# Performance work log

Hardware: AMD Instinct MI355X
Metric: run time of the kernel (lower is better)

Reference implementation:

```python
import jax, jax.numpy as jnp
import numpy as np

HEADS = 8
DIM_HEAD = 64


def setup_inputs() -> dict:
    key = jax.random.key(0)
    ks = jax.random.split(key, 5)
    dim = 512
    dim_inner = HEADS * DIM_HEAD
    return {
        "fmap": jax.random.normal(ks[0], (8, dim, 32, 32), dtype=jnp.float32),
        "gamma": jnp.ones((dim,), dtype=jnp.float32),
        "wq": jax.random.normal(ks[1], (dim_inner, dim), dtype=jnp.float32) * 0.05,
        "wv": jax.random.normal(ks[2], (dim_inner, dim), dtype=jnp.float32) * 0.05,
        "null_kv": jax.random.normal(ks[3], (2, HEADS, DIM_HEAD), dtype=jnp.float32),
        "wo": jax.random.normal(ks[4], (dim, dim_inner), dtype=jnp.float32) * 0.05,
    }


def reference(fmap, gamma, wq, wv, null_kv, wo):
    b, c, H, W = fmap.shape
    h, d = HEADS, DIM_HEAD
    n = H * W
    scale = d ** (-0.5)

    # ChannelRMSNorm: F.normalize over channel dim * sqrt(dim) * gamma
    l2 = jnp.sqrt(jnp.sum(fmap * fmap, axis=1, keepdims=True))
    x = fmap / jnp.maximum(l2, 1e-12) * (c ** 0.5) * gamma[None, :, None, None]

    # 1x1 convs as channel matmuls -> [b, h, n, d]
    def proj(w):
        t = jnp.einsum('bcxy,oc->boxy', x, w)          # [b, h*d, H, W]
        return t.reshape(b, h, d, n).transpose(0, 1, 3, 2)  # [b, h, n, d]

    q = proj(wq)
    v = proj(wv)
    k = q  # dot_product=False -> to_k is None, k = q

    # prepend null kv token
    nk = jnp.broadcast_to(null_kv[0][None, :, None, :], (b, h, 1, d))
    nv = jnp.broadcast_to(null_kv[1][None, :, None, :], (b, h, 1, d))
    k = jnp.concatenate([nk, k], axis=2)  # [b, h, n+1, d]
    v = jnp.concatenate([nv, v], axis=2)

    # negative squared L2 distance score: -(|q|^2 + |k|^2 - 2 q.k)
    q_sq = jnp.sum(q * q, axis=-1)  # [b, h, n]
    k_sq = jnp.sum(k * k, axis=-1)  # [b, h, n+1]
    qk = jnp.einsum('bhid,bhjd->bhij', q, k)
    sim = -(q_sq[..., :, None] + k_sq[..., None, :] - 2.0 * qk) * scale

    attn = jax.nn.softmax(sim, axis=-1)
    out = jnp.einsum('bhij,bhjd->bhid', attn, v)  # [b, h, n, d]

    out = out.transpose(0, 1, 3, 2).reshape(b, h * d, H, W)
    return jnp.einsum('boxy,co->bcxy', out, wo)
```

## Files before the change

kernel.cpp:

```cpp
#include <hip/hip_runtime.h>
#include <hip/hip_bf16.h>

#define DEV static __device__ __forceinline__

typedef __bf16 bf16x8 __attribute__((ext_vector_type(8)));
typedef float f32x4 __attribute__((ext_vector_type(4)));
typedef float f32x16 __attribute__((ext_vector_type(16)));
typedef unsigned u32x4 __attribute__((ext_vector_type(4)));
typedef unsigned short u16x8 __attribute__((ext_vector_type(8)));
typedef unsigned short u16x4 __attribute__((ext_vector_type(4)));

DEV unsigned short f2bf(float f) {
  unsigned u = __builtin_bit_cast(unsigned, f);
  u += 0x7fffu + ((u >> 16) & 1u);
  return (unsigned short)(u >> 16);
}
DEV float bf2f(unsigned short s) {
  return __builtin_bit_cast(float, (unsigned)s << 16);
}
DEV f32x4 mfma16(bf16x8 a, bf16x8 b, f32x4 c) {
  return __builtin_amdgcn_mfma_f32_16x16x32_bf16(a, b, c, 0, 0, 0);
}
DEV f32x16 mfma32(bf16x8 a, bf16x8 b, f32x16 c) {
  return __builtin_amdgcn_mfma_f32_32x32x16_bf16(a, b, c, 0, 0, 0);
}
DEV bf16x8 ld8(const unsigned short* p) {
  return __builtin_bit_cast(bf16x8, *(const u16x8*)p);
}
DEV void gload16(const unsigned short* g, unsigned short* l) {
  auto* g1 = reinterpret_cast<const __attribute__((address_space(1))) unsigned int*>(
      reinterpret_cast<uintptr_t>(g));
  auto* l3 = reinterpret_cast<__attribute__((address_space(3))) unsigned int*>(
      reinterpret_cast<uintptr_t>(l));
  __builtin_amdgcn_global_load_lds(g1, l3, 16, 0, 0);
}

__global__ __launch_bounds__(256) void prep_k(const float* __restrict__ fmap,
                                              const float* __restrict__ gamma,
                                              const float* __restrict__ wq,
                                              const float* __restrict__ wv,
                                              const float* __restrict__ wo,
                                              unsigned short* __restrict__ xt,
                                              unsigned short* __restrict__ wqb,
                                              unsigned short* __restrict__ wvb,
                                              unsigned short* __restrict__ wob) {
  int bid = blockIdx.x, tid = threadIdx.x;
  if (bid >= 256) {
    int t4 = bid - 256;
    int g = t4 >> 5;
    const float* src = (g == 0) ? wq : (g == 1) ? wv : wo;
    unsigned short* dst = (g == 0) ? wqb : (g == 1) ? wvb : wob;
    int base = (t4 & 31) * 1024 + tid;
    const float4* s = (const float4*)src;
#pragma unroll
    for (int i = 0; i < 4; ++i) {
      int idx = base + i * 256;
      float4 a = s[idx * 2], b = s[idx * 2 + 1];
      u16x8 o;
      o[0] = f2bf(a.x); o[1] = f2bf(a.y); o[2] = f2bf(a.z); o[3] = f2bf(a.w);
      o[4] = f2bf(b.x); o[5] = f2bf(b.y); o[6] = f2bf(b.z); o[7] = f2bf(b.w);
      ((u16x8*)dst)[idx] = o;
    }
    return;
  }
  __shared__ float slab[512][33];
  __shared__ float psum[32][33];
  __shared__ float rn_l[32];
  __shared__ float gl[512];
  int b = bid >> 5, n0 = (bid & 31) * 32;
  gl[tid] = gamma[tid];
  gl[tid + 256] = gamma[tid + 256];
  int q = tid & 7, cg = tid >> 3;
  int n4 = q * 4;
  float s0 = 0.f, s1 = 0.f, s2 = 0.f, s3 = 0.f;
  const float* pb = fmap + ((size_t)(b * 512 + cg * 16)) * 1024 + n0 + n4;
#pragma unroll
  for (int i = 0; i < 16; ++i) {
    float4 v = *(const float4*)(pb + (size_t)i * 1024);
    int c = cg * 16 + i;
    slab[c][n4] = v.x; slab[c][n4 + 1] = v.y; slab[c][n4 + 2] = v.z; slab[c][n4 + 3] = v.w;
    s0 += v.x * v.x; s1 += v.y * v.y; s2 += v.z * v.z; s3 += v.w * v.w;
  }
  psum[cg][n4] = s0; psum[cg][n4 + 1] = s1; psum[cg][n4 + 2] = s2; psum[cg][n4 + 3] = s3;
  __syncthreads();
  if (tid < 32) {
    float ts = 0.f;
#pragma unroll
    for (int k = 0; k < 32; ++k) ts += psum[k][tid];
    rn_l[tid] = 22.62741699796952f / fmaxf(sqrtf(ts), 1e-12f);
  }
  __syncthreads();
  int nn = tid >> 3, cc = tid & 7;
  float sc = rn_l[nn];
#pragma unroll
  for (int c0 = 0; c0 < 512; c0 += 64) {
    u16x8 o;
#pragma unroll
    for (int e = 0; e < 8; ++e) {
      int c = c0 + cc * 8 + e;
      o[e] = f2bf(slab[c][nn] * sc * gl[c]);
    }
    *(u16x8*)(xt + ((size_t)(b * 1024 + n0 + nn)) * 512 + c0 + cc * 8) = o;
  }
}

__global__ __launch_bounds__(512) void gemm_qv_k(const unsigned short* __restrict__ A,
                                                 const unsigned short* __restrict__ wqb,
                                                 const unsigned short* __restrict__ wvb,
                                                 const float* __restrict__ nkv,
                                                 unsigned short* __restrict__ QF,
                                                 unsigned short* __restrict__ VF,
                                                 float* __restrict__ qsqs,
                                                 float* __restrict__ p0g) {
  __shared__ unsigned short a_lds[2][128 * 64];
  __shared__ unsigned short bq_lds[2][128 * 64];
  __shared__ unsigned short bv_lds[2][128 * 64];
  int tid = threadIdx.x, lane = tid & 63, wid = tid >> 6;
  int isV = wid >> 2, gw = wid & 3;
  int wr = gw >> 1, wc = gw & 1;
  int m0 = blockIdx.y * 128, n0 = blockIdx.x * 128;
  int srow = (lane >> 3);
  int scol = ((lane & 7) ^ ((lane >> 3) & 7)) * 8;
  f32x4 acc[4][4] = {};

#define QV_STAGE(BUF, KT)                                                          \
  {                                                                                \
    int il0 = wid * 2;                                                             \
    _Pragma("unroll")                                                              \
    for (int i = 0; i < 2; ++i) {                                                  \
      int il = il0 + i;                                                            \
      gload16(A + (size_t)(m0 + il * 8 + srow) * 512 + (KT) + scol, &a_lds[BUF][il * 512]);   \
      gload16(wqb + (size_t)(n0 + il * 8 + srow) * 512 + (KT) + scol, &bq_lds[BUF][il * 512]); \
      gload16(wvb + (size_t)(n0 + il * 8 + srow) * 512 + (KT) + scol, &bv_lds[BUF][il * 512]); \
    }                                                                              \
  }

  QV_STAGE(0, 0)
  asm volatile("s_waitcnt vmcnt(0)" ::: "memory");
  __syncthreads();
  int cur = 0;
#pragma unroll 1
  for (int t = 0; t < 8; ++t) {
    if (t < 7) QV_STAGE(cur ^ 1, (t + 1) * 64)
    const unsigned short* al = &a_lds[cur][0];
    const unsigned short* bl = isV ? &bv_lds[cur][0] : &bq_lds[cur][0];
#pragma unroll
    for (int ks = 0; ks < 2; ++ks) {
      int c = ks * 4 + (lane >> 4);
      int cs = (c ^ (lane & 7)) * 8;
      bf16x8 af[4], bfr[4];
#pragma unroll
      for (int rt = 0; rt < 4; ++rt)
        af[rt] = ld8(&al[(wr * 64 + rt * 16 + (lane & 15)) * 64 + cs]);
#pragma unroll
      for (int ct = 0; ct < 4; ++ct)
        bfr[ct] = ld8(&bl[(wc * 64 + ct * 16 + (lane & 15)) * 64 + cs]);
#pragma unroll
      for (int rt = 0; rt < 4; ++rt)
#pragma unroll
        for (int ct = 0; ct < 4; ++ct)
          acc[rt][ct] = mfma16(af[rt], bfr[ct], acc[rt][ct]);
    }
    asm volatile("s_waitcnt vmcnt(0)" ::: "memory");
    __syncthreads();
    cur ^= 1;
  }
  if (!isV) {
    const float COEF = 0.18033688011112042f;
    int head = blockIdx.x * 2 + wc;
    const float* nk = nkv + head * 64;
    float nk_own[4], nks = 0.f;
#pragma unroll
    for (int ct = 0; ct < 4; ++ct) {
      nk_own[ct] = nk[ct * 16 + (lane & 15)];
      nks += nk_own[ct] * nk_own[ct];
    }
    nks += __shfl_xor(nks, 1); nks += __shfl_xor(nks, 2);
    nks += __shfl_xor(nks, 4); nks += __shfl_xor(nks, 8);
#pragma unroll
    for (int rt = 0; rt < 4; ++rt)
#pragma unroll
      for (int r = 0; r < 4; ++r) {
        float qs = 0.f, dot = 0.f;
        unsigned short qr[4];
#pragma unroll
        for (int ct = 0; ct < 4; ++ct) {
          unsigned short us = f2bf(acc[rt][ct][r]);
          qr[ct] = us;
          float v = bf2f(us);
          qs += v * v;
          dot += v * nk_own[ct];
        }
        int n = m0 + wr * 64 + rt * 16 + (lane >> 4) * 4 + r;
        int bb = n >> 10, nl = n & 1023;
        int bh = bb * 8 + head;
        size_t fidx = (size_t)(bh * 32 + (nl >> 5)) * 2048 + (nl & 31) * 16 + (lane & 15);
#pragma unroll
        for (int ct = 0; ct < 4; ++ct) QF[fidx + ct * 512] = qr[ct];
        qs += __shfl_xor(qs, 1); qs += __shfl_xor(qs, 2);
        qs += __shfl_xor(qs, 4); qs += __shfl_xor(qs, 8);
        dot += __shfl_xor(dot, 1); dot += __shfl_xor(dot, 2);
        dot += __shfl_xor(dot, 4); dot += __shfl_xor(dot, 8);
        if ((lane & 15) == 0) {
          qsqs[bh * 1024 + nl] = qs * COEF;
          p0g[bh * 1024 + nl] = __builtin_amdgcn_exp2f((2.f * dot - nks) * COEF);
        }
      }
  } else {
#pragma unroll
    for (int rt = 0; rt < 4; ++rt)
#pragma unroll
      for (int ct = 0; ct < 4; ++ct) {
        int nb = m0 + wr * 64 + rt * 16 + (lane >> 4) * 4;
        int o = n0 + wc * 64 + ct * 16 + (lane & 15);
        int b = nb >> 10, j = nb & 1023;
        int h = o >> 6, d = o & 63;
        int bh = b * 8 + h;
        size_t idx = (size_t)(bh * 32 + (j >> 5)) * 2048 + ((j >> 4) & 1) * 1024 + (d >> 5) * 512 +
                     (d & 31) * 16 + (j & 15);
        u16x4 pk;
#pragma unroll
        for (int r = 0; r < 4; ++r) pk[r] = f2bf(acc[rt][ct][r]);
        *(u16x4*)(VF + idx) = pk;
      }
  }
}

__global__ __launch_bounds__(256) void gemm_o_k(const unsigned short* __restrict__ A,
                                                const unsigned short* __restrict__ Bt,
                                                float* __restrict__ Cp) {
  __shared__ unsigned short a_lds[2][64 * 64];
  __shared__ unsigned short b_lds[2][128 * 64];
  int bid = blockIdx.x;
  int y = (bid >> 3) & 7;
  int x = (bid & 7) + ((bid >> 6) << 3);
  int m0 = y * 64, n0 = x * 128;
  int tid = threadIdx.x, lane = tid & 63, wid = tid >> 6;
  int wr = wid >> 1, wc = wid & 1;
  int srow = (lane >> 3);
  int scol = ((lane & 7) ^ ((lane >> 3) & 7)) * 8;
  f32x4 acc[2][4] = {};

#define O_STAGE(BUF, KT)                                                           \
  {                                                                                \
    _Pragma("unroll")                                                              \
    for (int i = 0; i < 2; ++i) {                                                  \
      int il = wid * 2 + i;                                                        \
      gload16(A + (size_t)(m0 + il * 8 + srow) * 512 + (KT) + scol, &a_lds[BUF][il * 512]);    \
    }                                                                              \
    _Pragma("unroll")                                                              \
    for (int i = 0; i < 4; ++i) {                                                  \
      int il = wid * 4 + i;                                                        \
      gload16(Bt + (size_t)(n0 + il * 8 + srow) * 512 + (KT) + scol, &b_lds[BUF][il * 512]);   \
    }                                                                              \
  }

  O_STAGE(0, 0)
  asm volatile("s_waitcnt vmcnt(0)" ::: "memory");
  __syncthreads();
  int cur = 0;
#pragma unroll 1
  for (int t = 0; t < 8; ++t) {
    if (t < 7) O_STAGE(cur ^ 1, (t + 1) * 64)
    const unsigned short* al = &a_lds[cur][0];
    const unsigned short* bl = &b_lds[cur][0];
#pragma unroll
    for (int ks = 0; ks < 2; ++ks) {
      int c = ks * 4 + (lane >> 4);
      int cs = (c ^ (lane & 7)) * 8;
      bf16x8 af[2], bfr[4];
#pragma unroll
      for (int rt = 0; rt < 2; ++rt)
        af[rt] = ld8(&al[(wr * 32 + rt * 16 + (lane & 15)) * 64 + cs]);
#pragma unroll
      for (int ct = 0; ct < 4; ++ct)
        bfr[ct] = ld8(&bl[(wc * 64 + ct * 16 + (lane & 15)) * 64 + cs]);
#pragma unroll
      for (int rt = 0; rt < 2; ++rt)
#pragma unroll
        for (int ct = 0; ct < 4; ++ct)
          acc[rt][ct] = mfma16(af[rt], bfr[ct], acc[rt][ct]);
    }
    asm volatile("s_waitcnt vmcnt(0)" ::: "memory");
    __syncthreads();
    cur ^= 1;
  }
  int bb = n0 >> 10;
#pragma unroll
  for (int rt = 0; rt < 2; ++rt)
#pragma unroll
    for (int ct = 0; ct < 4; ++ct)
#pragma unroll
      for (int r = 0; r < 4; ++r) {
        int row = m0 + wr * 32 + rt * 16 + (lane >> 4) * 4 + r;
        int col = (n0 & 1023) + wc * 64 + ct * 16 + (lane & 15);
        Cp[((size_t)(bb * 512 + row)) * 1024 + col] = acc[rt][ct][r];
      }
}

__global__ __launch_bounds__(512) void attn_k(const unsigned short* __restrict__ QF,
                                              const unsigned short* __restrict__ VF,
                                              const float* __restrict__ qsqs,
                                              const float* __restrict__ p0g,
                                              const float* __restrict__ nkv,
                                              unsigned short* __restrict__ att) {
  const float C2 = 0.36067376022224085f;
  int bid = blockIdx.x;
  int s0 = bid >> 3;
  int bh = ((bid & 7) << 3) | (s0 & 7);
  int qt = s0 >> 3;
  int b = bh >> 3, h = bh & 7;
  int n0 = qt * 128;
  int tid = threadIdx.x, lane = tid & 63, wid = tid >> 6;
  int wq = wid & 3, jg = wid >> 2;
  int l31 = lane & 31, hi = lane >> 5;

  __shared__ float ob_l[32][4][64];
  __shared__ float dsb[4][32];
  __shared__ float p0_l[128];
  __shared__ float nv_l[64];
  __shared__ float dn_l[4][32];

  if (tid < 128) p0_l[tid] = p0g[bh * 1024 + n0 + tid];
  else if (tid < 192) nv_l[tid - 128] = nkv[512 + h * 64 + (tid - 128)];
  __syncthreads();

  bf16x8 qf[4];
  const unsigned short* qfp = QF + (size_t)(bh * 32 + qt * 4 + wq) * 2048 + l31 * 16 + hi * 8;
#pragma unroll
  for (int ks = 0; ks < 4; ++ks)
    qf[ks] = ld8(qfp + ks * 512);

  f32x16 oacc[2];
#pragma unroll
  for (int dh = 0; dh < 2; ++dh)
#pragma unroll
    for (int r = 0; r < 16; ++r) {
      int row = (r & 3) + 8 * (r >> 2) + 4 * hi;
      oacc[dh][r] = (jg == 0) ? p0_l[wq * 32 + row] * nv_l[dh * 32 + l31] : 0.f;
    }

  f32x4 dsum4 = {0.f, 0.f, 0.f, 0.f};
  const unsigned short* kbase = QF + (size_t)bh * 65536 + l31 * 16 + hi * 8;
  const unsigned short* vbase = VF + (size_t)bh * 65536 + l31 * 16 + hi * 8;
  const float* ksb = qsqs + bh * 1024 + 4 * hi;

  bf16x8 kfA[4], kfB[4], vfA[2][2], vfB[2][2];
  f32x4 ksqA[4], ksqB[4];

#define LOADT(S, JT)                                                        \
  {                                                                         \
    const unsigned short* kp_ = kbase + (JT) * 2048;                        \
    kf##S[0] = ld8(kp_);        kf##S[1] = ld8(kp_ + 512);                  \
    kf##S[2] = ld8(kp_ + 1024); kf##S[3] = ld8(kp_ + 1536);                 \
    const unsigned short* vp_ = vbase + (JT) * 2048;                        \
    vf##S[0][0] = ld8(vp_);        vf##S[0][1] = ld8(vp_ + 1024);           \
    vf##S[1][0] = ld8(vp_ + 512);  vf##S[1][1] = ld8(vp_ + 1536);           \
    const float* kq_ = ksb + (JT) * 32;                                     \
    ksq##S[0] = *(const f32x4*)(kq_);      ksq##S[1] = *(const f32x4*)(kq_ + 8);  \
    ksq##S[2] = *(const f32x4*)(kq_ + 16); ksq##S[3] = *(const f32x4*)(kq_ + 24); \
  }

#define COMPT(S)                                                            \
  {                                                                         \
    f32x16 sa = {}, sb = {};                                                \
    __builtin_amdgcn_s_setprio(1);                                          \
    sa = mfma32(kf##S[0], qf[0], sa);                                       \
    sb = mfma32(kf##S[1], qf[1], sb);                                       \
    sa = mfma32(kf##S[2], qf[2], sa);                                       \
    sb = mfma32(kf##S[3], qf[3], sb);                                       \
    __builtin_amdgcn_s_setprio(0);                                          \
    float p[16];                                                            \
    _Pragma("unroll")                                                       \
    for (int r = 0; r < 16; ++r) {                                          \
      p[r] = __builtin_amdgcn_exp2f((sa[r] + sb[r]) * C2 - ksq##S[r >> 2][r & 3]);  \
      dsum4[r & 3] += p[r];                                                 \
    }                                                                       \
    unsigned w[4][2];                                                       \
    _Pragma("unroll")                                                       \
    for (int m = 0; m < 4; ++m) {                                           \
      asm("v_cvt_pk_bf16_f32 %0, %1, %2" : "=v"(w[m][0]) : "v"(p[4 * m]), "v"(p[4 * m + 1]));     \
      asm("v_cvt_pk_bf16_f32 %0, %1, %2" : "=v"(w[m][1]) : "v"(p[4 * m + 2]), "v"(p[4 * m + 3])); \
    }                                                                       \
    __builtin_amdgcn_s_setprio(1);                                          \
    _Pragma("unroll")                                                       \
    for (int sj = 0; sj < 2; ++sj) {                                        \
      unsigned a0 = w[2 * sj][0], b0 = w[2 * sj + 1][0];                    \
      unsigned a1 = w[2 * sj][1], b1 = w[2 * sj + 1][1];                    \
      asm("v_permlane32_swap_b32 %0, %1" : "+v"(a0), "+v"(b0));             \
      asm("v_permlane32_swap_b32 %0, %1" : "+v"(a1), "+v"(b1));             \
      u32x4 pw; pw[0] = a0; pw[1] = a1; pw[2] = b0; pw[3] = b1;             \
      bf16x8 pa = __builtin_bit_cast(bf16x8, pw);                           \
      oacc[0] = mfma32(pa, vf##S[0][sj], oacc[0]);                          \
      oacc[1] = mfma32(pa, vf##S[1][sj], oacc[1]);                          \
    }                                                                       \
    __builtin_amdgcn_s_setprio(0);                                          \
  }

  int jb = jg * 16;
  LOADT(A, jb)
#pragma unroll 1
  for (int s = 0; s < 7; ++s) {
    LOADT(B, jb + 2 * s + 1)
    COMPT(A)
    LOADT(A, jb + 2 * s + 2)
    COMPT(B)
  }
  LOADT(B, jb + 15)
  COMPT(A)
  COMPT(B)

  float dsum = (dsum4[0] + dsum4[1]) + (dsum4[2] + dsum4[3]);
  dsum += __shfl_xor(dsum, 32);

  if (jg == 1) {
#pragma unroll
    for (int dh = 0; dh < 2; ++dh)
#pragma unroll
      for (int r = 0; r < 16; ++r)
        ob_l[dh * 16 + r][wq][lane] = oacc[dh][r];
    if (hi == 0) dsb[wq][l31] = dsum;
  }
  __syncthreads();
  if (jg == 0) {
#pragma unroll
    for (int dh = 0; dh < 2; ++dh)
#pragma unroll
      for (int r = 0; r < 16; ++r)
        oacc[dh][r] += ob_l[dh * 16 + r][wq][lane];
    dsum += dsb[wq][l31] + p0_l[wq * 32 + l31];
    float rden = 1.0f / dsum;
    if (hi == 0) dn_l[wq][l31] = rden;
  }
  __syncthreads();

  if (jg == 0) {
#pragma unroll
    for (int dh = 0; dh < 2; ++dh)
#pragma unroll
      for (int r = 0; r < 16; ++r) {
        int row = (r & 3) + 8 * (r >> 2) + 4 * hi;
        float o = oacc[dh][r] * dn_l[wq][row];
        att[((size_t)(b * 1024 + n0 + wq * 32 + row)) * 512 + h * 64 + dh * 32 + l31] = f2bf(o);
      }
  }
}

extern "C" void kernel_launch(void* const* d_in, const int* in_sizes, int n_in,
                              void* d_out, int out_size, void* d_ws, size_t ws_size,
                              hipStream_t stream) {
  const float* fmap = (const float*)d_in[0];
  const float* gamma = (const float*)d_in[1];
  const float* wq = (const float*)d_in[2];
  const float* wv = (const float*)d_in[3];
  const float* nkv = (const float*)d_in[4];
  const float* wo = (const float*)d_in[5];
  float* out = (float*)d_out;

  const size_t M4 = (size_t)8192 * 512;
  unsigned short* x_t = (unsigned short*)d_ws;
  unsigned short* QF  = x_t + M4;
  unsigned short* VF  = QF + M4;
  unsigned short* att = VF + M4;
  unsigned short* wqb = att + M4;
  unsigned short* wvb = wqb + (size_t)512 * 512;
  unsigned short* wob = wvb + (size_t)512 * 512;
  float* qsqs = (float*)(wob + (size_t)512 * 512);
  float* p0g  = qsqs + 65536;

  prep_k<<<352, 256, 0, stream>>>(fmap, gamma, wq, wv, wo, x_t, wqb, wvb, wob);
  gemm_qv_k<<<dim3(4, 64), 512, 0, stream>>>(x_t, wqb, wvb, nkv, QF, VF, qsqs, p0g);
  attn_k<<<512, 512, 0, stream>>>(QF, VF, qsqs, p0g, nkv, att);
  gemm_o_k<<<512, 256, 0, stream>>>(wob, att, out);
}
```

Before: 66.16 us.

## Stage K/V tiles through LDS with direct global-to-LDS loads per chunk

Result: slower. 68.37 us (+3.3%).

```diff
diff --git a/kernel.cpp b/kernel.cpp
--- a/kernel.cpp
+++ b/kernel.cpp
@@ -315,6 +315,7 @@
   int wq = wid & 3, jg = wid >> 2;
   int l31 = lane & 31, hi = lane >> 5;
 
+  __shared__ unsigned short stage[32 * 512];
   __shared__ float ob_l[32][4][64];
   __shared__ float dsb[4][32];
   __shared__ float p0_l[128];
@@ -341,39 +342,47 @@
     }
 
   f32x4 dsum4 = {0.f, 0.f, 0.f, 0.f};
-  const unsigned short* kbase = QF + (size_t)bh * 65536 + l31 * 16 + hi * 8;
-  const unsigned short* vbase = VF + (size_t)bh * 65536 + l31 * 16 + hi * 8;
+  const unsigned short* kgbase = QF + (size_t)bh * 65536;
+  const unsigned short* vgbase = VF + (size_t)bh * 65536;
   const float* ksb = qsqs + bh * 1024 + 4 * hi;
 
-  bf16x8 kfA[4], kfB[4], vfA[2][2], vfB[2][2];
-  f32x4 ksqA[4], ksqB[4];
-
-#define LOADT(S, JT)                                                        \
+#define STAGE_CHUNK(C)                                                      \
   {                                                                         \
-    const unsigned short* kp_ = kbase + (JT) * 2048;                        \
-    kf##S[0] = ld8(kp_);        kf##S[1] = ld8(kp_ + 512);                  \
-    kf##S[2] = ld8(kp_ + 1024); kf##S[3] = ld8(kp_ + 1536);                 \
-    const unsigned short* vp_ = vbase + (JT) * 2048;                        \
-    vf##S[0][0] = ld8(vp_);        vf##S[0][1] = ld8(vp_ + 1024);           \
-    vf##S[1][0] = ld8(vp_ + 512);  vf##S[1][1] = ld8(vp_ + 1536);           \
+    _Pragma("unroll")                                                       \
+    for (int i = 0; i < 4; ++i) {                                           \
+      int s = wid * 4 + i;                                                  \
+      int sk = s & 15;                                                      \
+      int tile = (sk >> 3) * 16 + 2 * (C) + ((sk >> 2) & 1);                \
+      const unsigned short* src = ((s < 16) ? kgbase : vgbase) +            \
+          tile * 2048 + (sk & 3) * 512 + lane * 8;                          \
+      gload16(src, &stage[s * 512]);                                        \
+    }                                                                       \
+  }
+
+#define COMPT(TL, JT)                                                       \
+  {                                                                         \
+    const unsigned short* kp_ = &stage[(jg * 2 + (TL)) * 2048 + l31 * 16 + hi * 8]; \
+    bf16x8 kf0 = ld8(kp_), kf1 = ld8(kp_ + 512);                            \
+    bf16x8 kf2 = ld8(kp_ + 1024), kf3 = ld8(kp_ + 1536);                    \
+    const unsigned short* vp_ = &stage[(16 + jg * 2 + (TL)) * 512 * 4 / 4]; \
+    vp_ = &stage[16 * 512 + (jg * 2 + (TL)) * 2048 + l31 * 16 + hi * 8];    \
+    bf16x8 vf00 = ld8(vp_), vf01 = ld8(vp_ + 1024);                         \
+    bf16x8 vf10 = ld8(vp_ + 512), vf11 = ld8(vp_ + 1536);                   \
     const float* kq_ = ksb + (JT) * 32;                                     \
-    ksq##S[0] = *(const f32x4*)(kq_);      ksq##S[1] = *(const f32x4*)(kq_ + 8);  \
-    ksq##S[2] = *(const f32x4*)(kq_ + 16); ksq##S[3] = *(const f32x4*)(kq_ + 24); \
-  }
-
-#define COMPT(S)                                                            \
-  {                                                                         \
+    f32x4 ksq0 = *(const f32x4*)(kq_),      ksq1 = *(const f32x4*)(kq_ + 8);  \
+    f32x4 ksq2 = *(const f32x4*)(kq_ + 16), ksq3 = *(const f32x4*)(kq_ + 24); \
     f32x16 sa = {}, sb = {};                                                \
     __builtin_amdgcn_s_setprio(1);                                          \
-    sa = mfma32(kf##S[0], qf[0], sa);                                       \
-    sb = mfma32(kf##S[1], qf[1], sb);                                       \
-    sa = mfma32(kf##S[2], qf[2], sa);                                       \
-    sb = mfma32(kf##S[3], qf[3], sb);                                       \
+    sa = mfma32(kf0, qf[0], sa);                                            \
+    sb = mfma32(kf1, qf[1], sb);                                            \
+    sa = mfma32(kf2, qf[2], sa);                                            \
+    sb = mfma32(kf3, qf[3], sb);                                            \
     __builtin_amdgcn_s_setprio(0);                                          \
     float p[16];                                                            \
+    f32x4 ksqs[4] = {ksq0, ksq1, ksq2, ksq3};                               \
     _Pragma("unroll")                                                       \
     for (int r = 0; r < 16; ++r) {                                          \
-      p[r] = __builtin_amdgcn_exp2f((sa[r] + sb[r]) * C2 - ksq##S[r >> 2][r & 3]);  \
+      p[r] = __builtin_amdgcn_exp2f((sa[r] + sb[r]) * C2 - ksqs[r >> 2][r & 3]);  \
       dsum4[r & 3] += p[r];                                                 \
     }                                                                       \
     unsigned w[4][2];                                                       \
@@ -391,24 +400,22 @@
       asm("v_permlane32_swap_b32 %0, %1" : "+v"(a1), "+v"(b1));             \
       u32x4 pw; pw[0] = a0; pw[1] = a1; pw[2] = b0; pw[3] = b1;             \
       bf16x8 pa = __builtin_bit_cast(bf16x8, pw);                           \
-      oacc[0] = mfma32(pa, vf##S[0][sj], oacc[0]);                          \
-      oacc[1] = mfma32(pa, vf##S[1][sj], oacc[1]);                          \
+      oacc[0] = mfma32(pa, (sj == 0) ? vf00 : vf01, oacc[0]);               \
+      oacc[1] = mfma32(pa, (sj == 0) ? vf10 : vf11, oacc[1]);               \
     }                                                                       \
     __builtin_amdgcn_s_setprio(0);                                          \
   }
 
-  int jb = jg * 16;
-  LOADT(A, jb)
 #pragma unroll 1
-  for (int s = 0; s < 7; ++s) {
-    LOADT(B, jb + 2 * s + 1)
-    COMPT(A)
-    LOADT(A, jb + 2 * s + 2)
-    COMPT(B)
-  }
-  LOADT(B, jb + 15)
-  COMPT(A)
-  COMPT(B)
+  for (int c = 0; c < 8; ++c) {
+    STAGE_CHUNK(c)
+    asm volatile("s_waitcnt vmcnt(0)" ::: "memory");
+    __syncthreads();
+    int jt0 = jg * 16 + 2 * c;
+    COMPT(0, jt0)
+    COMPT(1, jt0 + 1)
+    __syncthreads();
+  }
 
   float dsum = (dsum4[0] + dsum4[1]) + (dsum4[2] + dsum4[3]);
   dsum += __shfl_xor(dsum, 32);
```
